# Kernel optimization log

Measured on AMD Instinct MI355X. Metric: run time of the kernel, lower is better.

## Reference

```python
import jax, jax.numpy as jnp
import numpy as np

NUM_HEADS = 14
SCALE = 0.125  # fixed constant in the source, not 1/sqrt(head_dim)
PATCH = 14
DIM = 3 * PATCH * PATCH  # 588


def setup_inputs() -> dict:
    key = jax.random.key(0)
    k_x, k_cw, k_cb, k_qw, k_qb = jax.random.split(key, 5)
    B, C_in, H, W = 8, 3, 448, 448
    x = jax.random.normal(k_x, (B, C_in, H, W), dtype=jnp.float32)
    # Conv2d(in_channels=3, dim, kernel=patch, stride=patch), torch layout OIHW
    fan_in = C_in * PATCH * PATCH
    bound = 1.0 / np.sqrt(fan_in)
    conv_w = jax.random.uniform(k_cw, (DIM, C_in, PATCH, PATCH), jnp.float32, -bound, bound)
    conv_b = jax.random.uniform(k_cb, (DIM,), jnp.float32, -bound, bound)
    # Linear(dim, 3*dim): weight [out, in] torch layout
    lb = 1.0 / np.sqrt(DIM)
    qkv_w = jax.random.uniform(k_qw, (3 * DIM, DIM), jnp.float32, -lb, lb)
    qkv_b = jax.random.uniform(k_qb, (3 * DIM,), jnp.float32, -lb, lb)
    return {"x": x, "conv_w": conv_w, "conv_b": conv_b, "qkv_w": qkv_w, "qkv_b": qkv_b}


def reference(x, conv_w, conv_b, qkv_w, qkv_b):
    # Patch embedding: conv kernel==stride==patch  -> [B, DIM, H/p, W/p]
    y = jax.lax.conv_general_dilated(
        x, conv_w, window_strides=(PATCH, PATCH), padding="VALID",
        dimension_numbers=("NCHW", "OIHW", "NCHW"))
    y = y + conv_b[None, :, None, None]
    B = y.shape[0]
    # flatten(2).transpose(1, 2) -> [B, N, C]
    tokens = y.reshape(B, DIM, -1).transpose(0, 2, 1)
    N, C = tokens.shape[1], tokens.shape[2]
    hd = C // NUM_HEADS  # 42
    qkv = tokens @ qkv_w.T + qkv_b  # [B, N, 3C]
    qkv = qkv.reshape(B, N, 3, NUM_HEADS, hd).transpose(2, 0, 3, 1, 4)  # [3,B,H,N,hd]
    q, k, v = qkv[0], qkv[1], qkv[2]
    attn = jnp.einsum("bhnd,bhmd->bhnm", q, k) * SCALE  # [B,H,N,N]
    attn = jax.nn.softmax(attn, axis=-1)
    out = jnp.einsum("bhnm,bhmd->bhnd", attn, v)  # [B,H,N,hd]
    out = out.transpose(0, 2, 1, 3).reshape(B, N, C)  # [B,N,C]
    return out
```

## Files before the change

kernel.cpp:

```cpp
#include <hip/hip_runtime.h>

typedef unsigned short u16;
typedef __attribute__((ext_vector_type(8))) short bf16x8;
typedef __attribute__((ext_vector_type(4))) float f32x4;

#define MTOK 8192
#define KP   640
#define CC   588
#define C3   1764
#define NH   14
#define SEQ  1024
#define HD   42
#define DP   64
#define DV   48

static __device__ __forceinline__ u16 f2b(float f) {
  unsigned u = __builtin_bit_cast(unsigned, f);
  u = (u + 0x7FFFu + ((u >> 16) & 1u)) >> 16;
  return (u16)u;
}

static __device__ __forceinline__ void gl_lds16(const void* g, void* l) {
  auto gp = (const unsigned int __attribute__((address_space(1)))*)((unsigned long long)g);
  auto lp = (unsigned int __attribute__((address_space(3)))*)((unsigned long long)l);
  __builtin_amdgcn_global_load_lds(gp, lp, 16, 0, 0);
}

__global__ void im2col_k(const float* __restrict__ x, u16* __restrict__ A) {
  int t = blockIdx.x;
  int b = t >> 10, pi = t & 1023, ph = pi >> 5, pw = pi & 31;
  const float* xb = x + (size_t)b * 3 * 448 * 448;
  for (int kk = threadIdx.x; kk < KP; kk += 256) {
    float v = 0.f;
    if (kk < CC) {
      int c = kk / 196, rem = kk - c * 196, i = rem / 14, j = rem - i * 14;
      v = xb[(size_t)(c * 448 + ph * 14 + i) * 448 + pw * 14 + j];
    }
    A[(size_t)t * KP + kk] = f2b(v);
  }
}

__global__ void padw_k(const float* __restrict__ w, u16* __restrict__ dst, int R) {
  int r = blockIdx.x;
  for (int c = threadIdx.x; c < KP; c += 256) {
    float v = (r < R && c < CC) ? w[(size_t)r * CC + c] : 0.f;
    dst[(size_t)r * KP + c] = f2b(v);
  }
}

template <int MODE>
__global__ void __launch_bounds__(256, 2) gemm_k(
    const u16* __restrict__ A, const u16* __restrict__ Bt,
    const float* __restrict__ bias, u16* __restrict__ out0,
    u16* __restrict__ qb, u16* __restrict__ kb, u16* __restrict__ vb) {
  __shared__ alignas(16) u16 sA[128 * 64];
  __shared__ alignas(16) u16 sB[128 * 64];
  const int tid = threadIdx.x;
  const int wave = tid >> 6, lane = tid & 63, quad = lane >> 4, l16 = lane & 15;
  const int wi = wave >> 1, wj = wave & 1;
  const int m0 = blockIdx.x * 128, n0 = blockIdx.y * 128;
  const int rL = lane >> 3, scid = lane & 7;
  const f32x4 z4 = {0.f, 0.f, 0.f, 0.f};

  f32x4 acc[4][4];
#pragma unroll
  for (int i = 0; i < 4; i++)
#pragma unroll
    for (int j = 0; j < 4; j++) acc[i][j] = z4;

  for (int k0 = 0; k0 < KP; k0 += 64) {
    __syncthreads();
#pragma unroll
    for (int cc = wave; cc < 16; cc += 4) {
      int r = cc * 8 + rL;
      int sch = scid ^ (r & 7);
      gl_lds16(A + ((size_t)(m0 + r) * KP + k0 + sch * 8), &sA[cc * 512]);
    }
#pragma unroll
    for (int cc = wave; cc < 16; cc += 4) {
      int r = cc * 8 + rL;
      int sch = scid ^ (r & 7);
      gl_lds16(Bt + ((size_t)(n0 + r) * KP + k0 + sch * 8), &sB[cc * 512]);
    }
    __syncthreads();
#pragma unroll
    for (int ks = 0; ks < 2; ks++) {
      bf16x8 af[4], bfr[4];
#pragma unroll
      for (int i = 0; i < 4; i++) {
        int r = wi * 64 + i * 16 + l16;
        int ch = (ks * 4 + quad) ^ (r & 7);
        af[i] = *(const bf16x8*)&sA[r * 64 + ch * 8];
      }
#pragma unroll
      for (int j = 0; j < 4; j++) {
        int r = wj * 64 + j * 16 + l16;
        int ch = (ks * 4 + quad) ^ (r & 7);
        bfr[j] = *(const bf16x8*)&sB[r * 64 + ch * 8];
      }
#pragma unroll
      for (int i = 0; i < 4; i++)
#pragma unroll
        for (int j = 0; j < 4; j++)
          acc[i][j] = __builtin_amdgcn_mfma_f32_16x16x32_bf16(af[i], bfr[j], acc[i][j], 0, 0, 0);
    }
  }

  const int baser = wi * 64 + quad * 4;
  if (MODE == 0) {
#pragma unroll
    for (int j = 0; j < 4; j++) {
      int col = n0 + wj * 64 + j * 16 + l16;
      float bs = (col < CC) ? bias[col] : 0.f;
#pragma unroll
      for (int i = 0; i < 4; i++) {
        int row = m0 + baser + i * 16;
#pragma unroll
        for (int r = 0; r < 4; r++)
          out0[(size_t)(row + r) * KP + col] = f2b(acc[i][j][r] + bs);
      }
    }
  } else {
#pragma unroll
    for (int j = 0; j < 4; j++) {
      int col = n0 + wj * 64 + j * 16 + l16;
      if (col < C3) {
        float bs = bias[col];
        int which = col / CC;
        int rem = col - which * CC;
        int h = rem / HD;
        int d = rem - h * HD;
        u16* dst = (which == 0) ? qb : (which == 1) ? kb : vb;
#pragma unroll
        for (int i = 0; i < 4; i++) {
          int row = m0 + baser + i * 16;
#pragma unroll
          for (int r = 0; r < 4; r++) {
            int rw = row + r;
            int b = rw >> 10, n = rw & 1023;
            dst[((size_t)((b * NH + h) * SEQ + n)) * DP + d] = f2b(acc[i][j][r] + bs);
          }
        }
      }
    }
  }
}

__global__ void vtrans_k(const u16* __restrict__ vb, u16* __restrict__ vT) {
  __shared__ u16 tile[64 * 49];
  int bh = blockIdx.x, mt = blockIdx.y;
  for (int idx = threadIdx.x; idx < 64 * DV; idx += 256) {
    int n = idx / DV, d = idx - n * DV;
    u16 v = 0;
    if (d < HD) v = vb[((size_t)(bh * SEQ + mt * 64 + n)) * DP + d];
    tile[n * 49 + d] = v;
  }
  __syncthreads();
  for (int idx = threadIdx.x; idx < DV * 64; idx += 256) {
    int d = idx >> 6, n = idx & 63;
    u16 v = (d < HD) ? tile[n * 49 + d] : ((d == HD) ? (u16)0x3F80 : (u16)0);
    vT[((size_t)(bh * DV + d)) * SEQ + mt * 64 + n] = v;
  }
}

__global__ void __launch_bounds__(256, 2) attn_k(
    const u16* __restrict__ qb, const u16* __restrict__ kb,
    const u16* __restrict__ vT, float* __restrict__ out) {
  __shared__ alignas(16) u16 sK[64 * 64];
  __shared__ alignas(16) u16 sV[DV * 64];
  __shared__ alignas(16) u16 sP[64 * 72];
  const int tid = threadIdx.x;
  const int wave = tid >> 6, lane = tid & 63, quad = lane >> 4, l16 = lane & 15;
  const int bh = blockIdx.x >> 4, qt = blockIdx.x & 15;
  const int q0 = qt * 64;
  const int rL = lane >> 3, scid = lane & 7;
  const float SC2 = 0.18033688011112042f;
  const f32x4 z4 = {0.f, 0.f, 0.f, 0.f};

  bf16x8 aq0, aq1;
  {
    const u16* qrow = qb + ((size_t)(bh * SEQ + q0 + wave * 16 + l16)) * DP;
    aq0 = *(const bf16x8*)&qrow[quad * 8];
    aq1 = *(const bf16x8*)&qrow[32 + quad * 8];
  }
  f32x4 o[3] = {z4, z4, z4};
  const u16* kb0 = kb + (size_t)bh * SEQ * DP;
  const u16* vb0 = vT + (size_t)bh * DV * SEQ;

  for (int kt = 0; kt < 16; kt++) {
    const int m0 = kt * 64;
    __syncthreads();
    {
      const u16* ktile = kb0 + (size_t)m0 * DP;
#pragma unroll
      for (int cc = wave; cc < 8; cc += 4) {
        int r = cc * 8 + rL;
        int sch = scid ^ (r & 7);
        gl_lds16(ktile + ((size_t)r * 64 + sch * 8), &sK[cc * 512]);
      }
      for (int cc = wave; cc < 6; cc += 4) {
        int d = cc * 8 + rL;
        int sch = scid ^ (d & 7);
        gl_lds16(vb0 + ((size_t)d * SEQ + m0 + sch * 8), &sV[cc * 512]);
      }
    }
    __syncthreads();
#pragma unroll
    for (int j = 0; j < 4; j++) {
      f32x4 s = z4;
#pragma unroll
      for (int ks = 0; ks < 2; ks++) {
        int n = j * 16 + l16;
        int ch = (ks * 4 + quad) ^ (n & 7);
        bf16x8 bk = *(const bf16x8*)&sK[n * 64 + ch * 8];
        s = __builtin_amdgcn_mfma_f32_16x16x32_bf16(ks == 0 ? aq0 : aq1, bk, s, 0, 0, 0);
      }
#pragma unroll
      for (int r = 0; r < 4; r++) {
        float p = __builtin_amdgcn_exp2f(s[r] * SC2);
        sP[(wave * 16 + quad * 4 + r) * 72 + j * 16 + l16] = f2b(p);
      }
    }
    __syncthreads();
#pragma unroll
    for (int ks = 0; ks < 2; ks++) {
      bf16x8 ap = *(const bf16x8*)&sP[(wave * 16 + l16) * 72 + ks * 32 + quad * 8];
#pragma unroll
      for (int j = 0; j < 3; j++) {
        int d = j * 16 + l16;
        int ch = (ks * 4 + quad) ^ (d & 7);
        bf16x8 bv = *(const bf16x8*)&sV[d * 64 + ch * 8];
        o[j] = __builtin_amdgcn_mfma_f32_16x16x32_bf16(ap, bv, o[j], 0, 0, 0);
      }
    }
  }
  __syncthreads();
  float* lsum = (float*)sP;
  if (l16 == 10) {
#pragma unroll
    for (int r = 0; r < 4; r++) lsum[wave * 16 + quad * 4 + r] = o[2][r];
  }
  __syncthreads();
  const int b = bh / NH, h = bh - b * NH;
#pragma unroll
  for (int r = 0; r < 4; r++) {
    int row = wave * 16 + quad * 4 + r;
    float rc = 1.f / lsum[row];
    float* orow = out + ((size_t)(b * SEQ + q0 + row)) * CC + h * HD;
#pragma unroll
    for (int j = 0; j < 3; j++) {
      int d = j * 16 + l16;
      if (d < HD) orow[d] = o[j][r] * rc;
    }
  }
}

extern "C" void kernel_launch(void* const* d_in, const int* in_sizes, int n_in,
                              void* d_out, int out_size, void* d_ws, size_t ws_size,
                              hipStream_t stream) {
  (void)in_sizes; (void)n_in; (void)out_size; (void)ws_size;
  const float* x      = (const float*)d_in[0];
  const float* conv_w = (const float*)d_in[1];
  const float* conv_b = (const float*)d_in[2];
  const float* qkv_w  = (const float*)d_in[3];
  const float* qkv_b  = (const float*)d_in[4];
  float* out = (float*)d_out;

  char* ws = (char*)d_ws;
  size_t off = 0;
  u16* A      = (u16*)(ws + off); off += (size_t)MTOK * KP * 2;
  u16* Wc     = (u16*)(ws + off); off += (size_t)640 * KP * 2;
  u16* Wq     = (u16*)(ws + off); off += (size_t)1792 * KP * 2;
  u16* tokens = (u16*)(ws + off); off += (size_t)MTOK * KP * 2;
  u16* qbuf   = (u16*)(ws + off); off += (size_t)112 * SEQ * DP * 2;
  u16* kbuf   = (u16*)(ws + off); off += (size_t)112 * SEQ * DP * 2;
  u16* vbuf   = (u16*)(ws + off); off += (size_t)112 * SEQ * DP * 2;
  u16* vTb    = (u16*)(ws + off); off += (size_t)112 * DV * SEQ * 2;

  hipMemsetAsync(qbuf, 0, (size_t)3 * 112 * SEQ * DP * 2, stream);
  im2col_k<<<MTOK, 256, 0, stream>>>(x, A);
  padw_k<<<640, 256, 0, stream>>>(conv_w, Wc, CC);
  padw_k<<<1792, 256, 0, stream>>>(qkv_w, Wq, C3);
  gemm_k<0><<<dim3(64, 5), 256, 0, stream>>>(A, Wc, conv_b, tokens, nullptr, nullptr, nullptr);
  gemm_k<1><<<dim3(64, 14), 256, 0, stream>>>(tokens, Wq, qkv_b, nullptr, qbuf, kbuf, vbuf);
  vtrans_k<<<dim3(112, 16), 256, 0, stream>>>(vbuf, vTb);
  attn_k<<<112 * 16, 256, 0, stream>>>(qbuf, kbuf, vTb, out);
}
```

Baseline: 208.1 us.

## Enlarge attention query tile to 256 rows per block with register-blocked MFMA

The attention kernel now has each wave handle 64 query rows (four 16-row subtiles) instead of 16. Each K/V tile loaded into LDS is therefore reused across four times as many queries, and the grid shrinks from 1792 blocks to 448. Block indices are remapped so that neighbouring blocks work on different heads. The barrier between the P write and the PV MFMAs is removed because each wave reads only its own P rows. The workspace memset now clears only the K buffer, which relies on the Q padding columns being finite. The change adds register pressure (48 accumulators plus 8 Q fragments), uses more LDS, and 448 blocks may leave parts of the GPU underused.

```diff
diff --git a/kernel.cpp b/kernel.cpp
--- a/kernel.cpp
+++ b/kernel.cpp
@@ -168,22 +168,31 @@
     const u16* __restrict__ vT, float* __restrict__ out) {
   __shared__ alignas(16) u16 sK[64 * 64];
   __shared__ alignas(16) u16 sV[DV * 64];
-  __shared__ alignas(16) u16 sP[64 * 72];
+  __shared__ alignas(16) u16 sP[256 * 72];
+  __shared__ float lbuf[256];
   const int tid = threadIdx.x;
   const int wave = tid >> 6, lane = tid & 63, quad = lane >> 4, l16 = lane & 15;
-  const int bh = blockIdx.x >> 4, qt = blockIdx.x & 15;
-  const int q0 = qt * 64;
+  const int g = blockIdx.x;
+  const int bh = (g & 7) * 14 + (g >> 5);
+  const int qt = (g >> 3) & 3;
+  const int q0 = qt * 256;
   const int rL = lane >> 3, scid = lane & 7;
   const float SC2 = 0.18033688011112042f;
   const f32x4 z4 = {0.f, 0.f, 0.f, 0.f};
-
-  bf16x8 aq0, aq1;
-  {
-    const u16* qrow = qb + ((size_t)(bh * SEQ + q0 + wave * 16 + l16)) * DP;
-    aq0 = *(const bf16x8*)&qrow[quad * 8];
-    aq1 = *(const bf16x8*)&qrow[32 + quad * 8];
-  }
-  f32x4 o[3] = {z4, z4, z4};
+  const int prow = wave * 64;
+
+  bf16x8 aq[4][2];
+#pragma unroll
+  for (int i = 0; i < 4; i++) {
+    const u16* qrow = qb + ((size_t)(bh * SEQ + q0 + wave * 64 + i * 16 + l16)) * DP;
+    aq[i][0] = *(const bf16x8*)&qrow[quad * 8];
+    aq[i][1] = *(const bf16x8*)&qrow[32 + quad * 8];
+  }
+  f32x4 o[4][3];
+#pragma unroll
+  for (int i = 0; i < 4; i++)
+#pragma unroll
+    for (int j = 0; j < 3; j++) o[i][j] = z4;
   const u16* kb0 = kb + (size_t)bh * SEQ * DP;
   const u16* vb0 = vT + (size_t)bh * DV * SEQ;
 
@@ -195,62 +204,75 @@
 #pragma unroll
       for (int cc = wave; cc < 8; cc += 4) {
         int r = cc * 8 + rL;
-        int sch = scid ^ (r & 7);
-        gl_lds16(ktile + ((size_t)r * 64 + sch * 8), &sK[cc * 512]);
-      }
+        gl_lds16(ktile + ((size_t)r * 64 + (scid ^ (r & 7)) * 8), &sK[cc * 512]);
+      }
+#pragma unroll
       for (int cc = wave; cc < 6; cc += 4) {
         int d = cc * 8 + rL;
-        int sch = scid ^ (d & 7);
-        gl_lds16(vb0 + ((size_t)d * SEQ + m0 + sch * 8), &sV[cc * 512]);
+        gl_lds16(vb0 + ((size_t)d * SEQ + m0 + (scid ^ (d & 7)) * 8), &sV[cc * 512]);
       }
     }
     __syncthreads();
+    bf16x8 bk[4][2];
 #pragma unroll
     for (int j = 0; j < 4; j++) {
-      f32x4 s = z4;
-#pragma unroll
-      for (int ks = 0; ks < 2; ks++) {
-        int n = j * 16 + l16;
-        int ch = (ks * 4 + quad) ^ (n & 7);
-        bf16x8 bk = *(const bf16x8*)&sK[n * 64 + ch * 8];
-        s = __builtin_amdgcn_mfma_f32_16x16x32_bf16(ks == 0 ? aq0 : aq1, bk, s, 0, 0, 0);
-      }
-#pragma unroll
-      for (int r = 0; r < 4; r++) {
-        float p = __builtin_amdgcn_exp2f(s[r] * SC2);
-        sP[(wave * 16 + quad * 4 + r) * 72 + j * 16 + l16] = f2b(p);
-      }
-    }
-    __syncthreads();
+      int n = j * 16 + l16;
+#pragma unroll
+      for (int ks = 0; ks < 2; ks++)
+        bk[j][ks] = *(const bf16x8*)&sK[n * 64 + (((ks * 4 + quad) ^ (n & 7)) * 8)];
+    }
+#pragma unroll
+    for (int i = 0; i < 4; i++) {
+#pragma unroll
+      for (int j = 0; j < 4; j++) {
+        f32x4 s = z4;
+        s = __builtin_amdgcn_mfma_f32_16x16x32_bf16(aq[i][0], bk[j][0], s, 0, 0, 0);
+        s = __builtin_amdgcn_mfma_f32_16x16x32_bf16(aq[i][1], bk[j][1], s, 0, 0, 0);
+#pragma unroll
+        for (int r = 0; r < 4; r++)
+          sP[(prow + i * 16 + quad * 4 + r) * 72 + j * 16 + l16] =
+              f2b(__builtin_amdgcn_exp2f(s[r] * SC2));
+      }
+    }
 #pragma unroll
     for (int ks = 0; ks < 2; ks++) {
-      bf16x8 ap = *(const bf16x8*)&sP[(wave * 16 + l16) * 72 + ks * 32 + quad * 8];
+      bf16x8 bv[3];
 #pragma unroll
       for (int j = 0; j < 3; j++) {
         int d = j * 16 + l16;
-        int ch = (ks * 4 + quad) ^ (d & 7);
-        bf16x8 bv = *(const bf16x8*)&sV[d * 64 + ch * 8];
-        o[j] = __builtin_amdgcn_mfma_f32_16x16x32_bf16(ap, bv, o[j], 0, 0, 0);
+        bv[j] = *(const bf16x8*)&sV[d * 64 + (((ks * 4 + quad) ^ (d & 7)) * 8)];
+      }
+#pragma unroll
+      for (int i = 0; i < 4; i++) {
+        bf16x8 ap = *(const bf16x8*)&sP[(prow + i * 16 + l16) * 72 + ks * 32 + quad * 8];
+#pragma unroll
+        for (int j = 0; j < 3; j++)
+          o[i][j] = __builtin_amdgcn_mfma_f32_16x16x32_bf16(ap, bv[j], o[i][j], 0, 0, 0);
       }
     }
   }
   __syncthreads();
-  float* lsum = (float*)sP;
   if (l16 == 10) {
 #pragma unroll
-    for (int r = 0; r < 4; r++) lsum[wave * 16 + quad * 4 + r] = o[2][r];
+    for (int i = 0; i < 4; i++)
+#pragma unroll
+      for (int r = 0; r < 4; r++)
+        lbuf[prow + i * 16 + quad * 4 + r] = o[i][2][r];
   }
   __syncthreads();
   const int b = bh / NH, h = bh - b * NH;
 #pragma unroll
-  for (int r = 0; r < 4; r++) {
-    int row = wave * 16 + quad * 4 + r;
-    float rc = 1.f / lsum[row];
-    float* orow = out + ((size_t)(b * SEQ + q0 + row)) * CC + h * HD;
-#pragma unroll
-    for (int j = 0; j < 3; j++) {
-      int d = j * 16 + l16;
-      if (d < HD) orow[d] = o[j][r] * rc;
+  for (int i = 0; i < 4; i++) {
+#pragma unroll
+    for (int r = 0; r < 4; r++) {
+      int row = prow + i * 16 + quad * 4 + r;
+      float rc = 1.f / lbuf[row];
+      float* orow = out + ((size_t)(b * SEQ + q0 + row)) * CC + h * HD;
+#pragma unroll
+      for (int j = 0; j < 3; j++) {
+        int d = j * 16 + l16;
+        if (d < HD) orow[d] = o[i][j][r] * rc;
+      }
     }
   }
 }
@@ -277,12 +299,12 @@
   u16* vbuf   = (u16*)(ws + off); off += (size_t)112 * SEQ * DP * 2;
   u16* vTb    = (u16*)(ws + off); off += (size_t)112 * DV * SEQ * 2;
 
-  hipMemsetAsync(qbuf, 0, (size_t)3 * 112 * SEQ * DP * 2, stream);
+  hipMemsetAsync(kbuf, 0, (size_t)112 * SEQ * DP * 2, stream);
   im2col_k<<<MTOK, 256, 0, stream>>>(x, A);
   padw_k<<<640, 256, 0, stream>>>(conv_w, Wc, CC);
   padw_k<<<1792, 256, 0, stream>>>(qkv_w, Wq, C3);
   gemm_k<0><<<dim3(64, 5), 256, 0, stream>>>(A, Wc, conv_b, tokens, nullptr, nullptr, nullptr);
   gemm_k<1><<<dim3(64, 14), 256, 0, stream>>>(tokens, Wq, qkv_b, nullptr, qbuf, kbuf, vbuf);
   vtrans_k<<<dim3(112, 16), 256, 0, stream>>>(vbuf, vTb);
-  attn_k<<<112 * 16, 256, 0, stream>>>(qbuf, kbuf, vTb, out);
-}
+  attn_k<<<448, 256, 0, stream>>>(qbuf, kbuf, vTb, out);
+}
```

Result: faster. 193.4 us (-7.1%).
